# Performance work log

Hardware: AMD Instinct MI355X
Metric: run time of the kernel (lower is better)

The kernel has to match this reference:

```python
import jax, jax.numpy as jnp
import numpy as np

OUT = 7  # adaptive max-pool output size (7x7)


def setup_inputs() -> dict:
    key = jax.random.key(0)
    k1, k2, k3, k4, k5, k6 = jax.random.split(key, 6)
    C, H, W = 512, 50, 50          # feature map (stride-16 backbone)
    h_img, w_img = 800, 800        # original image
    N = 256                        # number of ROIs
    x = jax.random.normal(k1, (1, C, H, W), dtype=jnp.float32)
    img = jax.random.normal(k2, (1, 3, h_img, w_img), dtype=jnp.float32)
    # rois: (x0, y0, w, h) in image coordinates, guaranteed in-bounds
    x0 = jax.random.uniform(k3, (N,), minval=0.0, maxval=0.5 * w_img)
    y0 = jax.random.uniform(k4, (N,), minval=0.0, maxval=0.5 * h_img)
    rw = jax.random.uniform(k5, (N,), minval=0.1 * w_img, maxval=0.45 * w_img)
    rh = jax.random.uniform(k6, (N,), minval=0.1 * h_img, maxval=0.45 * h_img)
    rois = jnp.stack([x0, y0, rw, rh], axis=1).astype(jnp.float32)
    return {"x": x, "img": img, "rois": rois}


def _ceil_div(a, b):
    return -((-a) // b)


def reference(x, img, rois):
    # Faithful to the torch module: scale rois to feature grid, truncate to int,
    # crop x[:, ry:ry+rh+1, rx:rx+rw+1] and AdaptiveMaxPool2d to 7x7.
    # AdaptiveMaxPool2d bin i over size s: [floor(i*s/OUT), ceil((i+1)*s/OUT)).
    _, C, H, W = x.shape
    h_img, w_img = img.shape[2], img.shape[3]
    wscale = W / w_img
    hscale = H / h_img
    rx = (rois[:, 0] * wscale).astype(jnp.int32)
    ry = (rois[:, 1] * hscale).astype(jnp.int32)
    rw = (rois[:, 2] * wscale).astype(jnp.int32)
    rh = (rois[:, 3] * hscale).astype(jnp.int32)
    sh = rh + 1  # crop height per ROI
    sw = rw + 1  # crop width per ROI
    N = rois.shape[0]
    p = jnp.arange(OUT)
    # per-ROI, per-bin start/end (half-open) in feature coords: [N, OUT]
    ys = ry[:, None] + (p[None, :] * sh[:, None]) // OUT
    ye = ry[:, None] + _ceil_div((p[None, :] + 1) * sh[:, None], OUT)
    xs = rx[:, None] + (p[None, :] * sw[:, None]) // OUT
    xe = rx[:, None] + _ceil_div((p[None, :] + 1) * sw[:, None], OUT)

    feat = x[0]  # [C, H, W]
    neg = jnp.array(-jnp.inf, dtype=x.dtype)

    # ---- pass 1: max over rows within each vertical bin ----
    Kh = H // OUT + 3  # max possible bin height
    kh = jnp.arange(Kh)
    row_idx = ys[:, :, None] + kh  # [N, OUT, Kh]
    valid_y = row_idx < ye[:, :, None]
    row_idx = jnp.minimum(row_idx, H - 1)
    g = feat[:, row_idx, :]  # [C, N, OUT, Kh, W]
    g = jnp.where(valid_y[None, :, :, :, None], g, neg)
    rowmax = g.max(axis=3)                 # [C, N, OUT, W]
    rowmax = jnp.moveaxis(rowmax, 0, 1)    # [N, C, OUT, W]

    # ---- pass 2: max over columns within each horizontal bin ----
    Kw = W // OUT + 3
    kw = jnp.arange(Kw)
    col_idx = xs[:, :, None] + kw  # [N, OUT, Kw]
    valid_x = col_idx < xe[:, :, None]
    col_idx = jnp.minimum(col_idx, W - 1)
    flat = col_idx.reshape(N, 1, 1, OUT * Kw)
    g2 = jnp.take_along_axis(rowmax, flat, axis=3)  # [N, C, OUT, OUT*Kw]
    g2 = g2.reshape(N, C, OUT, OUT, Kw)
    g2 = jnp.where(valid_x[:, None, None, :, :], g2, neg)
    return g2.max(axis=4)  # [N, C, OUT, OUT]
```

## Files before the change

kernel.cpp:

```cpp
#include <hip/hip_runtime.h>

#define CCH  512
#define HF   50
#define WF   50
#define NROI 256
#define WS_NEEDED (HF * WF * CCH * sizeof(float))
#define ROWSTR (WF * 256)
#define OBSTR 258

__global__ __launch_bounds__(256) void transpose_kernel(
    const float* __restrict__ x, float* __restrict__ xt)
{
    __shared__ float tile[64][51];
    const int y  = blockIdx.x >> 3;
    const int c0 = (blockIdx.x & 7) << 6;
    const int t  = threadIdx.x;
    const int wv = t >> 6, lane = t & 63;

    for (int r = 0; r < 16; ++r) {
        const int cl = wv * 16 + r;
        if (lane < WF)
            tile[cl][lane] = x[(c0 + cl) * (HF * WF) + y * WF + lane];
    }
    __syncthreads();

    const int g   = c0 >> 8;
    const int cin = c0 & 255;
    for (int k = 0; k < 13; ++k) {
        const int xx = (t >> 6) + 4 * k;
        if (xx < WF)
            xt[((size_t)g * (HF * WF) + y * WF + xx) * 256 + cin + (t & 63)]
                = tile[t & 63][xx];
    }
}

__global__ __launch_bounds__(512, 4) void roipool_t_kernel(
    const float* __restrict__ xt,
    const float* __restrict__ rois,
    float* __restrict__ out)
{
    __shared__ float ob[49 * OBSTR];

    const int n  = blockIdx.x >> 1;
    const int cg = blockIdx.x & 1;
    const int t  = threadIdx.x;
    const int wv = t >> 6, lane = t & 63;

    const float4 rv = *(const float4*)(rois + n * 4);
    const int rx = (int)(rv.x * 0.0625f);
    const int ry = (int)(rv.y * 0.0625f);
    const int sw = (int)(rv.z * 0.0625f) + 1;
    const int sh = (int)(rv.w * 0.0625f) + 1;

    const float* part = xt + (size_t)cg * (HF * WF * 256) + 4 * lane;

#define M4(a) { m.x = fmaxf(m.x,(a).x); m.y = fmaxf(m.y,(a).y); \
                m.z = fmaxf(m.z,(a).z); m.w = fmaxf(m.w,(a).w); }
#define LD(k) (*(const float4*)(rp + (k) * 256))

    for (int task = wv; task < 49; task += 8) {
        const int ph = task / 7;
        const int pw = task - ph * 7;
        const int ys = ry + (ph * sh) / 7;
        const int ye = ry + ((ph + 1) * sh + 6) / 7;
        const int xs = rx + (pw * sw) / 7;
        const int xe = rx + ((pw + 1) * sw + 6) / 7;
        const int yspan = ye - ys;
        const int xspan = xe - xs;
        const float* rp = part + (ys * WF + xs) * 256;

        float4 m = make_float4(-INFINITY, -INFINITY, -INFINITY, -INFINITY);
        switch (xspan) {
        case 1: {
            float4 a0 = LD(0);
            for (int y = 1; y < yspan; ++y) {
                rp += ROWSTR; float4 b0 = LD(0);
                M4(a0); a0 = b0;
            }
            M4(a0);
        } break;
        case 2: {
            float4 a0 = LD(0), a1 = LD(1);
            for (int y = 1; y < yspan; ++y) {
                rp += ROWSTR; float4 b0 = LD(0), b1 = LD(1);
                M4(a0); M4(a1); a0 = b0; a1 = b1;
            }
            M4(a0); M4(a1);
        } break;
        case 3: {
            float4 a0 = LD(0), a1 = LD(1), a2 = LD(2);
            for (int y = 1; y < yspan; ++y) {
                rp += ROWSTR; float4 b0 = LD(0), b1 = LD(1), b2 = LD(2);
                M4(a0); M4(a1); M4(a2); a0 = b0; a1 = b1; a2 = b2;
            }
            M4(a0); M4(a1); M4(a2);
        } break;
        case 4: {
            float4 a0 = LD(0), a1 = LD(1), a2 = LD(2), a3 = LD(3);
            for (int y = 1; y < yspan; ++y) {
                rp += ROWSTR; float4 b0 = LD(0), b1 = LD(1), b2 = LD(2), b3 = LD(3);
                M4(a0); M4(a1); M4(a2); M4(a3);
                a0 = b0; a1 = b1; a2 = b2; a3 = b3;
            }
            M4(a0); M4(a1); M4(a2); M4(a3);
        } break;
        default: {
            float4 a0 = LD(0), a1 = LD(1), a2 = LD(2), a3 = LD(3), a4 = LD(4);
            for (int y = 1; y < yspan; ++y) {
                rp += ROWSTR; float4 b0 = LD(0), b1 = LD(1), b2 = LD(2), b3 = LD(3), b4 = LD(4);
                M4(a0); M4(a1); M4(a2); M4(a3); M4(a4);
                a0 = b0; a1 = b1; a2 = b2; a3 = b3; a4 = b4;
            }
            M4(a0); M4(a1); M4(a2); M4(a3); M4(a4);
        } break;
        }

        *(float2*)&ob[task * OBSTR + 4 * lane]     = make_float2(m.x, m.y);
        *(float2*)&ob[task * OBSTR + 4 * lane + 2] = make_float2(m.z, m.w);
    }
#undef LD
#undef M4
    __syncthreads();

    float* op = out + (size_t)(n * CCH + cg * 256) * 49;
    int c = t / 49, task = t - c * 49;
    for (int i = t; i < 256 * 49; i += 512) {
        __builtin_nontemporal_store(ob[task * OBSTR + c], &op[i]);
        task += 22; c += 10;
        if (task >= 49) { task -= 49; c += 1; }
    }
}

__global__ __launch_bounds__(256) void roipool_direct(
    const float* __restrict__ x, const float* __restrict__ rois,
    float* __restrict__ out, int total)
{
    const int stride = gridDim.x * blockDim.x;
    for (int idx = blockIdx.x * blockDim.x + threadIdx.x; idx < total; idx += stride) {
        int n = idx / (CCH * 49), rem = idx - n * (CCH * 49);
        int c = rem / 49, pp = rem - c * 49;
        int ph = pp / 7, pw = pp - ph * 7;
        const float* r = rois + n * 4;
        int rx = (int)(r[0] * 0.0625f), ry = (int)(r[1] * 0.0625f);
        int sw = (int)(r[2] * 0.0625f) + 1, sh = (int)(r[3] * 0.0625f) + 1;
        int ys = ry + (ph * sh) / 7, ye = ry + ((ph + 1) * sh + 6) / 7;
        int xs = rx + (pw * sw) / 7, xe = rx + ((pw + 1) * sw + 6) / 7;
        const float* f = x + c * (HF * WF);
        float m = -INFINITY;
        for (int y = ys; y < ye; ++y)
            for (int xx = xs; xx < xe; ++xx)
                m = fmaxf(m, f[y * WF + xx]);
        out[idx] = m;
    }
}

extern "C" void kernel_launch(void* const* d_in, const int* in_sizes, int n_in,
                              void* d_out, int out_size, void* d_ws, size_t ws_size,
                              hipStream_t stream) {
    const float* x    = (const float*)d_in[0];
    const float* rois = (const float*)d_in[2];
    float* out = (float*)d_out;

    if (ws_size >= WS_NEEDED) {
        float* xt = (float*)d_ws;
        transpose_kernel<<<HF * 8, 256, 0, stream>>>(x, xt);
        roipool_t_kernel<<<NROI * 2, 512, 0, stream>>>(xt, rois, out);
    } else {
        const int total = NROI * CCH * 49;
        roipool_direct<<<2048, 256, 0, stream>>>(x, rois, out, total);
    }
}
```

Baseline: 25.71 us.

## Use persistent 1024-thread blocks with atomic work queue for ROI items

The pooling kernel becomes persistent: 256 blocks of 1024 threads pull (roi, channel-half) items from a global atomic counter, which the transpose kernel resets. This is meant to balance the uneven per-ROI work and cut block launch and tail overhead. In exchange it adds atomics and extra block-wide barriers per item. The larger blocks can also lower occupancy, and the 49 bins spread over 16 waves leave some waves idle.

```diff
diff --git a/kernel.cpp b/kernel.cpp
--- a/kernel.cpp
+++ b/kernel.cpp
@@ -4,13 +4,17 @@
 #define HF   50
 #define WF   50
 #define NROI 256
-#define WS_NEEDED (HF * WF * CCH * sizeof(float))
+#define XT_BYTES (HF * WF * CCH * sizeof(float))
+#define WS_NEEDED (XT_BYTES + 64)
 #define ROWSTR (WF * 256)
 #define OBSTR 258
+#define ITEMS (NROI * 2)
 
 __global__ __launch_bounds__(256) void transpose_kernel(
-    const float* __restrict__ x, float* __restrict__ xt)
+    const float* __restrict__ x, float* __restrict__ xt, int* __restrict__ cnt)
 {
+    if (blockIdx.x == 0 && threadIdx.x == 0) cnt[0] = 0;
+
     __shared__ float tile[64][51];
     const int y  = blockIdx.x >> 3;
     const int c0 = (blockIdx.x & 7) << 6;
@@ -34,101 +38,119 @@
     }
 }
 
-__global__ __launch_bounds__(512, 4) void roipool_t_kernel(
+__global__ __launch_bounds__(1024, 4) void roipool_t_kernel(
     const float* __restrict__ xt,
     const float* __restrict__ rois,
-    float* __restrict__ out)
+    float* __restrict__ out,
+    int* __restrict__ cnt)
 {
     __shared__ float ob[49 * OBSTR];
+    __shared__ int s_item;
 
-    const int n  = blockIdx.x >> 1;
-    const int cg = blockIdx.x & 1;
     const int t  = threadIdx.x;
     const int wv = t >> 6, lane = t & 63;
 
-    const float4 rv = *(const float4*)(rois + n * 4);
-    const int rx = (int)(rv.x * 0.0625f);
-    const int ry = (int)(rv.y * 0.0625f);
-    const int sw = (int)(rv.z * 0.0625f) + 1;
-    const int sh = (int)(rv.w * 0.0625f) + 1;
-
-    const float* part = xt + (size_t)cg * (HF * WF * 256) + 4 * lane;
+    if (t == 0) s_item = atomicAdd(cnt, 1);
+    __syncthreads();
+    int item = s_item;
 
 #define M4(a) { m.x = fmaxf(m.x,(a).x); m.y = fmaxf(m.y,(a).y); \
                 m.z = fmaxf(m.z,(a).z); m.w = fmaxf(m.w,(a).w); }
 #define LD(k) (*(const float4*)(rp + (k) * 256))
 
-    for (int task = wv; task < 49; task += 8) {
-        const int ph = task / 7;
-        const int pw = task - ph * 7;
-        const int ys = ry + (ph * sh) / 7;
-        const int ye = ry + ((ph + 1) * sh + 6) / 7;
-        const int xs = rx + (pw * sw) / 7;
-        const int xe = rx + ((pw + 1) * sw + 6) / 7;
-        const int yspan = ye - ys;
-        const int xspan = xe - xs;
-        const float* rp = part + (ys * WF + xs) * 256;
+    while (item < ITEMS) {
+        if (t == 0) s_item = atomicAdd(cnt, 1);
 
-        float4 m = make_float4(-INFINITY, -INFINITY, -INFINITY, -INFINITY);
-        switch (xspan) {
-        case 1: {
-            float4 a0 = LD(0);
-            for (int y = 1; y < yspan; ++y) {
-                rp += ROWSTR; float4 b0 = LD(0);
-                M4(a0); a0 = b0;
+        const int n  = item >> 1;
+        const int cg = item & 1;
+
+        const float4 rv = *(const float4*)(rois + n * 4);
+        const int rx = (int)(rv.x * 0.0625f);
+        const int ry = (int)(rv.y * 0.0625f);
+        const int sw = (int)(rv.z * 0.0625f) + 1;
+        const int sh = (int)(rv.w * 0.0625f) + 1;
+        const float* part = xt + (size_t)cg * (HF * WF * 256) + 4 * lane;
+
+        for (int task = wv; task < 49; task += 16) {
+            const int ph = task / 7;
+            const int pw = task - ph * 7;
+            const int ys = ry + (ph * sh) / 7;
+            const int ye = ry + ((ph + 1) * sh + 6) / 7;
+            const int xs = rx + (pw * sw) / 7;
+            const int xe = rx + ((pw + 1) * sw + 6) / 7;
+            const int yspan = ye - ys;
+            const int xspan = xe - xs;
+            const float* rp = part + (ys * WF + xs) * 256;
+
+            float4 m = make_float4(-INFINITY, -INFINITY, -INFINITY, -INFINITY);
+            switch (xspan) {
+            case 1: {
+                float4 a0 = LD(0);
+                for (int y = 1; y < yspan; ++y) {
+                    rp += ROWSTR; float4 b0 = LD(0);
+                    M4(a0); a0 = b0;
+                }
+                M4(a0);
+            } break;
+            case 2: {
+                float4 a0 = LD(0), a1 = LD(1);
+                for (int y = 1; y < yspan; ++y) {
+                    rp += ROWSTR; float4 b0 = LD(0), b1 = LD(1);
+                    M4(a0); M4(a1); a0 = b0; a1 = b1;
+                }
+                M4(a0); M4(a1);
+            } break;
+            case 3: {
+                float4 a0 = LD(0), a1 = LD(1), a2 = LD(2);
+                for (int y = 1; y < yspan; ++y) {
+                    rp += ROWSTR; float4 b0 = LD(0), b1 = LD(1), b2 = LD(2);
+                    M4(a0); M4(a1); M4(a2); a0 = b0; a1 = b1; a2 = b2;
+                }
+                M4(a0); M4(a1); M4(a2);
+            } break;
+            case 4: {
+                float4 a0 = LD(0), a1 = LD(1), a2 = LD(2), a3 = LD(3);
+                for (int y = 1; y < yspan; ++y) {
+                    rp += ROWSTR; float4 b0 = LD(0), b1 = LD(1), b2 = LD(2), b3 = LD(3);
+                    M4(a0); M4(a1); M4(a2); M4(a3);
+                    a0 = b0; a1 = b1; a2 = b2; a3 = b3;
+                }
+                M4(a0); M4(a1); M4(a2); M4(a3);
+            } break;
+            default: {
+                float4 a0 = LD(0), a1 = LD(1), a2 = LD(2), a3 = LD(3), a4 = LD(4);
+                for (int y = 1; y < yspan; ++y) {
+                    rp += ROWSTR; float4 b0 = LD(0), b1 = LD(1), b2 = LD(2), b3 = LD(3), b4 = LD(4);
+                    M4(a0); M4(a1); M4(a2); M4(a3); M4(a4);
+                    a0 = b0; a1 = b1; a2 = b2; a3 = b3; a4 = b4;
+                }
+                M4(a0); M4(a1); M4(a2); M4(a3); M4(a4);
+            } break;
             }
-            M4(a0);
-        } break;
-        case 2: {
-            float4 a0 = LD(0), a1 = LD(1);
-            for (int y = 1; y < yspan; ++y) {
-                rp += ROWSTR; float4 b0 = LD(0), b1 = LD(1);
-                M4(a0); M4(a1); a0 = b0; a1 = b1;
+
+            *(float2*)&ob[task * OBSTR + 4 * lane]     = make_float2(m.x, m.y);
+            *(float2*)&ob[task * OBSTR + 4 * lane + 2] = make_float2(m.z, m.w);
+        }
+        __syncthreads();
+        const int next = s_item;
+
+        float* op = out + (size_t)(n * CCH + cg * 256) * 49;
+        {
+            int c = t / 49, task = t - (t / 49) * 49;
+            #pragma unroll
+            for (int k = 0; k < 12; ++k) {
+                __builtin_nontemporal_store(ob[task * OBSTR + c], &op[t + k * 1024]);
+                task += 44; c += 20;
+                if (task >= 49) { task -= 49; c += 1; }
             }
-            M4(a0); M4(a1);
-        } break;
-        case 3: {
-            float4 a0 = LD(0), a1 = LD(1), a2 = LD(2);
-            for (int y = 1; y < yspan; ++y) {
-                rp += ROWSTR; float4 b0 = LD(0), b1 = LD(1), b2 = LD(2);
-                M4(a0); M4(a1); M4(a2); a0 = b0; a1 = b1; a2 = b2;
-            }
-            M4(a0); M4(a1); M4(a2);
-        } break;
-        case 4: {
-            float4 a0 = LD(0), a1 = LD(1), a2 = LD(2), a3 = LD(3);
-            for (int y = 1; y < yspan; ++y) {
-                rp += ROWSTR; float4 b0 = LD(0), b1 = LD(1), b2 = LD(2), b3 = LD(3);
-                M4(a0); M4(a1); M4(a2); M4(a3);
-                a0 = b0; a1 = b1; a2 = b2; a3 = b3;
-            }
-            M4(a0); M4(a1); M4(a2); M4(a3);
-        } break;
-        default: {
-            float4 a0 = LD(0), a1 = LD(1), a2 = LD(2), a3 = LD(3), a4 = LD(4);
-            for (int y = 1; y < yspan; ++y) {
-                rp += ROWSTR; float4 b0 = LD(0), b1 = LD(1), b2 = LD(2), b3 = LD(3), b4 = LD(4);
-                M4(a0); M4(a1); M4(a2); M4(a3); M4(a4);
-                a0 = b0; a1 = b1; a2 = b2; a3 = b3; a4 = b4;
-            }
-            M4(a0); M4(a1); M4(a2); M4(a3); M4(a4);
-        } break;
+            if (t < 256)
+                __builtin_nontemporal_store(ob[task * OBSTR + c], &op[t + 12 * 1024]);
         }
-
-        *(float2*)&ob[task * OBSTR + 4 * lane]     = make_float2(m.x, m.y);
-        *(float2*)&ob[task * OBSTR + 4 * lane + 2] = make_float2(m.z, m.w);
+        __syncthreads();
+        item = next;
     }
 #undef LD
 #undef M4
-    __syncthreads();
-
-    float* op = out + (size_t)(n * CCH + cg * 256) * 49;
-    int c = t / 49, task = t - c * 49;
-    for (int i = t; i < 256 * 49; i += 512) {
-        __builtin_nontemporal_store(ob[task * OBSTR + c], &op[i]);
-        task += 22; c += 10;
-        if (task >= 49) { task -= 49; c += 1; }
-    }
 }
 
 __global__ __launch_bounds__(256) void roipool_direct(
@@ -162,9 +184,10 @@
     float* out = (float*)d_out;
 
     if (ws_size >= WS_NEEDED) {
-        float* xt = (float*)d_ws;
-        transpose_kernel<<<HF * 8, 256, 0, stream>>>(x, xt);
-        roipool_t_kernel<<<NROI * 2, 512, 0, stream>>>(xt, rois, out);
+        float* xt  = (float*)d_ws;
+        int*   cnt = (int*)((char*)d_ws + XT_BYTES);
+        transpose_kernel<<<HF * 8, 256, 0, stream>>>(x, xt, cnt);
+        roipool_t_kernel<<<256, 1024, 0, stream>>>(xt, rois, out, cnt);
     } else {
         const int total = NROI * CCH * 49;
         roipool_direct<<<2048, 256, 0, stream>>>(x, rois, out, total);
```

Result: slower. 30.41 us (+18.3%).

## Fuse transpose and ROI pool into one kernel with a global atomic barrier

Applied to the files above, without the earlier changes.

Merges the channel-last transpose and the ROI max-pool kernels into a single launch. The first 400 blocks do the transpose and bump an atomic counter, then every block spins until all transpose units finish before pooling. The aim is to remove one kernel launch and the gap between kernels, at the cost of an extra memset launch and a grid-wide spin barrier. That barrier relies on all 512 blocks being co-resident, which the launch bounds allow.

```diff
diff --git a/kernel.cpp b/kernel.cpp
--- a/kernel.cpp
+++ b/kernel.cpp
@@ -4,47 +4,64 @@
 #define HF   50
 #define WF   50
 #define NROI 256
-#define WS_NEEDED (HF * WF * CCH * sizeof(float))
+#define XT_BYTES (HF * WF * CCH * sizeof(float))
+#define WS_NEEDED (XT_BYTES + 64)
 #define ROWSTR (WF * 256)
 #define OBSTR 258
+#define TUNITS (HF * 8)
 
-__global__ __launch_bounds__(256) void transpose_kernel(
-    const float* __restrict__ x, float* __restrict__ xt)
+__global__ __launch_bounds__(512, 4) void roipool_fused(
+    const float* __restrict__ x,
+    const float* __restrict__ rois,
+    float* __restrict__ out,
+    float* __restrict__ xt,
+    int* __restrict__ done)
 {
-    __shared__ float tile[64][51];
-    const int y  = blockIdx.x >> 3;
-    const int c0 = (blockIdx.x & 7) << 6;
-    const int t  = threadIdx.x;
-    const int wv = t >> 6, lane = t & 63;
+    __shared__ union {
+        float tile[64][51];
+        float ob[49 * OBSTR];
+    } sm;
 
-    for (int r = 0; r < 16; ++r) {
-        const int cl = wv * 16 + r;
-        if (lane < WF)
-            tile[cl][lane] = x[(c0 + cl) * (HF * WF) + y * WF + lane];
+    const int blk = blockIdx.x;
+    const int t   = threadIdx.x;
+    const int wv  = t >> 6, lane = t & 63;
+
+    if (blk < TUNITS) {
+        const int y  = blk >> 3;
+        const int c0 = (blk & 7) << 6;
+        if (t < 256) {
+            for (int r = 0; r < 16; ++r) {
+                const int cl = ((t >> 6) & 3) * 16 + r;
+                if (lane < WF)
+                    sm.tile[cl][lane] = x[(c0 + cl) * (HF * WF) + y * WF + lane];
+            }
+        }
+        __syncthreads();
+        if (t < 256) {
+            const int g   = c0 >> 8;
+            const int cin = c0 & 255;
+            for (int k = 0; k < 13; ++k) {
+                const int xx = ((t >> 6) & 3) + 4 * k;
+                if (xx < WF)
+                    xt[((size_t)g * (HF * WF) + y * WF + xx) * 256 + cin + lane]
+                        = sm.tile[lane][xx];
+            }
+        }
+        __syncthreads();
+        if (t == 0) {
+            __threadfence();
+            atomicAdd(done, 1);
+        }
+    }
+    if (t == 0) {
+        while (__hip_atomic_load(done, __ATOMIC_RELAXED, __HIP_MEMORY_SCOPE_AGENT) < TUNITS)
+            __builtin_amdgcn_s_sleep(4);
+        __threadfence();
     }
     __syncthreads();
 
-    const int g   = c0 >> 8;
-    const int cin = c0 & 255;
-    for (int k = 0; k < 13; ++k) {
-        const int xx = (t >> 6) + 4 * k;
-        if (xx < WF)
-            xt[((size_t)g * (HF * WF) + y * WF + xx) * 256 + cin + (t & 63)]
-                = tile[t & 63][xx];
-    }
-}
-
-__global__ __launch_bounds__(512, 4) void roipool_t_kernel(
-    const float* __restrict__ xt,
-    const float* __restrict__ rois,
-    float* __restrict__ out)
-{
-    __shared__ float ob[49 * OBSTR];
-
-    const int n  = blockIdx.x >> 1;
-    const int cg = blockIdx.x & 1;
-    const int t  = threadIdx.x;
-    const int wv = t >> 6, lane = t & 63;
+    const int n  = blk >> 1;
+    const int cg = blk & 1;
 
     const float4 rv = *(const float4*)(rois + n * 4);
     const int rx = (int)(rv.x * 0.0625f);
@@ -115,19 +132,21 @@
         } break;
         }
 
-        *(float2*)&ob[task * OBSTR + 4 * lane]     = make_float2(m.x, m.y);
-        *(float2*)&ob[task * OBSTR + 4 * lane + 2] = make_float2(m.z, m.w);
+        *(float2*)&sm.ob[task * OBSTR + 4 * lane]     = make_float2(m.x, m.y);
+        *(float2*)&sm.ob[task * OBSTR + 4 * lane + 2] = make_float2(m.z, m.w);
     }
 #undef LD
 #undef M4
     __syncthreads();
 
     float* op = out + (size_t)(n * CCH + cg * 256) * 49;
-    int c = t / 49, task = t - c * 49;
-    for (int i = t; i < 256 * 49; i += 512) {
-        __builtin_nontemporal_store(ob[task * OBSTR + c], &op[i]);
-        task += 22; c += 10;
-        if (task >= 49) { task -= 49; c += 1; }
+    {
+        int c = t / 49, task = t - (t / 49) * 49;
+        for (int i = t; i < 256 * 49; i += 512) {
+            __builtin_nontemporal_store(sm.ob[task * OBSTR + c], &op[i]);
+            task += 22; c += 10;
+            if (task >= 49) { task -= 49; c += 1; }
+        }
     }
 }
 
@@ -162,9 +181,10 @@
     float* out = (float*)d_out;
 
     if (ws_size >= WS_NEEDED) {
-        float* xt = (float*)d_ws;
-        transpose_kernel<<<HF * 8, 256, 0, stream>>>(x, xt);
-        roipool_t_kernel<<<NROI * 2, 512, 0, stream>>>(xt, rois, out);
+        float* xt  = (float*)d_ws;
+        int* done  = (int*)((char*)d_ws + XT_BYTES);
+        hipMemsetAsync(done, 0, sizeof(int), stream);
+        roipool_fused<<<512, 512, 0, stream>>>(x, rois, out, xt, done);
     } else {
         const int total = NROI * CCH * 49;
         roipool_direct<<<2048, 256, 0, stream>>>(x, rois, out, total);
```

Measured after the change: 72.77 us. 2.83x slower.
